# Kernel tuning notes

Hardware: AMD Instinct MI355X
Metric: run time of the kernel (lower is better)

The kernel has to match this reference:

```python
import jax, jax.numpy as jnp
import numpy as np

N = 100000      # nodes
E = 3_200_000   # edges
F_IN = 256      # input feature dim
R = 16          # rank_bound (GCN output dim)
D = 128         # embedding_dim (trans output)
B = 16384       # batch of node indices
EPS = 1e-5


def setup_inputs() -> dict:
    key = jax.random.key(0)
    ks = jax.random.split(key, 9)
    x = jax.random.normal(ks[0], (N, F_IN), jnp.float32)
    edge_index = jax.random.randint(ks[1], (2, E), 0, N, dtype=jnp.int64)
    trans = jax.random.normal(ks[2], (R, D), jnp.float32) * 0.1
    batch = jax.random.randint(ks[3], (B,), 0, N, dtype=jnp.int64)
    W = jax.random.normal(ks[4], (R, F_IN), jnp.float32) / np.sqrt(F_IN).astype(np.float32)
    b = jnp.zeros((R,), jnp.float32)
    ln_w = jnp.ones((R,), jnp.float32)
    ln_b = jnp.zeros((R,), jnp.float32)
    prelu_a = jnp.full((1,), 0.25, jnp.float32)  # PReLU single shared slope
    return dict(x=x, edge_index=edge_index, trans=trans, batch=batch,
                W=W, b=b, ln_w=ln_w, ln_b=ln_b, prelu_a=prelu_a)


def gcn_conv(x, edge_index, W, b):
    # PyG GCNConv: lin first, then symmetric-normalized aggregation with self-loops.
    h = x @ W.T  # [N, R]
    loop = jnp.arange(N, dtype=edge_index.dtype)
    src = jnp.concatenate([edge_index[0], loop])  # messages flow src -> dst
    dst = jnp.concatenate([edge_index[1], loop])
    deg = jax.ops.segment_sum(jnp.ones_like(dst, h.dtype), dst, num_segments=N)
    dinv = jnp.where(deg > 0, jax.lax.rsqrt(deg), 0.0)
    norm = dinv[src] * dinv[dst]                   # [E+N]
    msg = h[src] * norm[:, None]                   # gather [E+N, R]
    out = jax.ops.segment_sum(msg, dst, num_segments=N)  # scatter-add
    return out + b


def reference(x, edge_index, trans, batch, W, b, ln_w, ln_b, prelu_a):
    h = gcn_conv(x, edge_index, W, b)              # [N, R]
    # PyG LayerNorm (graph mode): normalize over all nodes and channels.
    h = h - h.mean()
    var = (h * h).mean()
    h = h * jax.lax.rsqrt(var + EPS) * ln_w + ln_b
    # PReLU
    h = jnp.where(h >= 0, h, prelu_a * h)
    emb = h @ trans                                # [N, D]
    return emb[batch]                              # index_select(0, batch)
```

## Files before the change

kernel.cpp:

```cpp
#include <hip/hip_runtime.h>

#define EPS 1e-5f
#define BSHIFT 8
#define BSIZE  256
#define NBMAX  512
#define PCHUNK 8192

__device__ __forceinline__ unsigned short f2bf(float f) {
    unsigned u = __float_as_uint(f);
    u += 0x7FFFu + ((u >> 16) & 1u);
    return (unsigned short)(u >> 16);
}
__device__ __forceinline__ float bf2f(unsigned short s) {
    return __uint_as_float(((unsigned)s) << 16);
}
__device__ __forceinline__ void acc8(float* acc, uint4 v) {
    acc[0] += bf2f((unsigned short)(v.x & 0xFFFFu)); acc[1] += bf2f((unsigned short)(v.x >> 16));
    acc[2] += bf2f((unsigned short)(v.y & 0xFFFFu)); acc[3] += bf2f((unsigned short)(v.y >> 16));
    acc[4] += bf2f((unsigned short)(v.z & 0xFFFFu)); acc[5] += bf2f((unsigned short)(v.z >> 16));
    acc[6] += bf2f((unsigned short)(v.w & 0xFFFFu)); acc[7] += bf2f((unsigned short)(v.w >> 16));
}

__global__ __launch_bounds__(512) void k_zero(unsigned* ghist, int NB) {
    int t = threadIdx.x;
    if (t < NB) ghist[t] = 0u;
}

__global__ __launch_bounds__(256) void k_bhist(const int* __restrict__ ei,
                                               unsigned* __restrict__ ghist, int E, int NB) {
    __shared__ unsigned sh[NBMAX];
    int t = threadIdx.x;
    for (int i = t; i < NB; i += 256) sh[i] = 0u;
    __syncthreads();
    const int4* dst4 = (const int4*)(ei + E);
    int E4 = E >> 2;
    int base4 = blockIdx.x * 1024;
#pragma unroll
    for (int i = 0; i < 4; i++) {
        int idx = base4 + i * 256 + t;
        if (idx < E4) {
            int4 d = dst4[idx];
            atomicAdd(&sh[d.x >> BSHIFT], 1u);
            atomicAdd(&sh[d.y >> BSHIFT], 1u);
            atomicAdd(&sh[d.z >> BSHIFT], 1u);
            atomicAdd(&sh[d.w >> BSHIFT], 1u);
        }
    }
    __syncthreads();
    for (int i = t; i < NB; i += 256) if (sh[i]) atomicAdd(&ghist[i], sh[i]);
}

__global__ __launch_bounds__(512) void k_bscan(const unsigned* __restrict__ ghist,
                                               unsigned* __restrict__ base,
                                               unsigned* __restrict__ cursor,
                                               unsigned* __restrict__ nstart,
                                               int NB, int N, int E) {
    __shared__ unsigned sh[512];
    int t = threadIdx.x;
    unsigned v = (t < NB) ? ghist[t] : 0u;
    sh[t] = v;
    __syncthreads();
    for (int off = 1; off < 512; off <<= 1) {
        unsigned a = (t >= off) ? sh[t - off] : 0u;
        __syncthreads();
        sh[t] += a;
        __syncthreads();
    }
    if (t < NB) { unsigned ex = sh[t] - v; base[t] = ex; cursor[t] = ex; }
    if (t == 0) { base[NB] = (unsigned)E; nstart[N] = (unsigned)E; }
}

__global__ __launch_bounds__(512) void k_bpart(const int* __restrict__ ei,
                                               unsigned* __restrict__ cursor,
                                               unsigned* __restrict__ sorted, int E, int NB) {
    __shared__ unsigned cnt[NBMAX];
    __shared__ unsigned lbase[NBMAX];
    __shared__ unsigned loff[NBMAX + 1];
    __shared__ unsigned sh[512];
    __shared__ unsigned stage[PCHUNK];
    __shared__ unsigned short bkt[PCHUNK];
    int t = threadIdx.x;
    for (int i = t; i < NB; i += 512) cnt[i] = 0u;
    __syncthreads();
    const int4* src4 = (const int4*)ei;
    const int4* dst4 = (const int4*)(ei + E);
    int E4 = E >> 2;
    int base4 = blockIdx.x * (PCHUNK / 4);
#pragma unroll
    for (int i = 0; i < PCHUNK / 4 / 512; i++) {
        int idx = base4 + i * 512 + t;
        if (idx < E4) {
            int4 d = dst4[idx];
            atomicAdd(&cnt[d.x >> BSHIFT], 1u);
            atomicAdd(&cnt[d.y >> BSHIFT], 1u);
            atomicAdd(&cnt[d.z >> BSHIFT], 1u);
            atomicAdd(&cnt[d.w >> BSHIFT], 1u);
        }
    }
    __syncthreads();
    unsigned v = (t < NB) ? cnt[t] : 0u;
    sh[t] = v;
    if (t < NB) lbase[t] = v ? atomicAdd(&cursor[t], v) : 0u;
    __syncthreads();
    for (int off = 1; off < 512; off <<= 1) {
        unsigned a = (t >= off) ? sh[t - off] : 0u;
        __syncthreads();
        sh[t] += a;
        __syncthreads();
    }
    if (t < NB) { loff[t] = sh[t] - v; cnt[t] = 0u; }
    if (t == NB - 1) loff[NB] = sh[t];
    __syncthreads();
    for (int b = t; b < NB; b += 512) {
        unsigned s = loff[b], e2 = loff[b + 1];
        for (unsigned j = s; j < e2; j++) bkt[j] = (unsigned short)b;
    }
#pragma unroll
    for (int i = 0; i < PCHUNK / 4 / 512; i++) {
        int idx = base4 + i * 512 + t;
        if (idx < E4) {
            int4 s = src4[idx];
            int4 d = dst4[idx];
            int b; unsigned r;
            b = d.x >> BSHIFT; r = atomicAdd(&cnt[b], 1u);
            stage[loff[b] + r] = (unsigned)s.x | ((unsigned)(d.x & (BSIZE - 1)) << 17);
            b = d.y >> BSHIFT; r = atomicAdd(&cnt[b], 1u);
            stage[loff[b] + r] = (unsigned)s.y | ((unsigned)(d.y & (BSIZE - 1)) << 17);
            b = d.z >> BSHIFT; r = atomicAdd(&cnt[b], 1u);
            stage[loff[b] + r] = (unsigned)s.z | ((unsigned)(d.z & (BSIZE - 1)) << 17);
            b = d.w >> BSHIFT; r = atomicAdd(&cnt[b], 1u);
            stage[loff[b] + r] = (unsigned)s.w | ((unsigned)(d.w & (BSIZE - 1)) << 17);
        }
    }
    __syncthreads();
    unsigned total = loff[NB];
    for (unsigned i = t; i < total; i += 512) {
        unsigned b = bkt[i];
        sorted[lbase[b] + (i - loff[b])] = stage[i];
    }
}

__global__ __launch_bounds__(256) void k_bdeg2(const unsigned* __restrict__ base,
                                               const unsigned* __restrict__ sorted,
                                               unsigned* __restrict__ nstart,
                                               float* __restrict__ dinv, int N) {
    __shared__ unsigned deg[BSIZE];
    int b = blockIdx.x, t = threadIdx.x;
    deg[t] = 0u;
    __syncthreads();
    unsigned s0 = base[b], s1 = base[b + 1];
    for (unsigned j = s0 + t; j < s1; j += 256)
        atomicAdd(&deg[sorted[j] >> 17], 1u);
    __syncthreads();
    unsigned d0 = deg[t];
    int lane = t & 63, wid = t >> 6;
    unsigned inc = d0;
    for (int off = 1; off < 64; off <<= 1) {
        unsigned u = __shfl_up(inc, off, 64);
        if (lane >= off) inc += u;
    }
    __shared__ unsigned wsum[4];
    if (lane == 63) wsum[wid] = inc;
    __syncthreads();
    unsigned wbase = 0;
    for (int w = 0; w < wid; w++) wbase += wsum[w];
    unsigned excl = wbase + inc - d0;
    int node = (b << BSHIFT) + t;
    if (node < N) {
        nstart[node] = s0 + excl;
        dinv[node] = rsqrtf((float)(d0 + 1u));
    }
}

__global__ __launch_bounds__(256) void k_bsort(const unsigned* __restrict__ base,
                                               const unsigned* __restrict__ nstart,
                                               const unsigned* __restrict__ sorted,
                                               unsigned* __restrict__ sorted2, int N) {
    __shared__ unsigned cur[BSIZE];
    int b = blockIdx.x, t = threadIdx.x;
    int node = (b << BSHIFT) + t;
    cur[t] = (node < N) ? nstart[node] : 0u;
    __syncthreads();
    unsigned s0 = base[b], s1 = base[b + 1];
    for (unsigned j = s0 + t; j < s1; j += 256) {
        unsigned u = sorted[j];
        unsigned pos = atomicAdd(&cur[u >> 17], 1u);
        sorted2[pos] = u & 0x1FFFFu;
    }
}

__global__ __launch_bounds__(256) void k_gemm(const float* __restrict__ x,
                                              const float* __restrict__ W,
                                              const float* __restrict__ dinv,
                                              unsigned short* __restrict__ hs, int N) {
    __shared__ float ws[16 * 256];
    int t = threadIdx.x;
    for (int i = t; i < 1024; i += 256) ((float4*)ws)[i] = ((const float4*)W)[i];
    __syncthreads();
    int node = blockIdx.x * 256 + t;
    if (node >= N) return;
    const float4* xr = (const float4*)(x + (size_t)node * 256);
    float acc[16];
#pragma unroll
    for (int r = 0; r < 16; r++) acc[r] = 0.f;
#pragma unroll 4
    for (int k = 0; k < 64; k++) {
        float4 a = xr[k];
#pragma unroll
        for (int r = 0; r < 16; r++) {
            float4 w = ((const float4*)ws)[r * 64 + k];
            acc[r] += a.x * w.x + a.y * w.y + a.z * w.z + a.w * w.w;
        }
    }
    float dv = dinv[node];
    unsigned pk[8];
#pragma unroll
    for (int i = 0; i < 8; i++)
        pk[i] = (unsigned)f2bf(acc[2 * i] * dv) | ((unsigned)f2bf(acc[2 * i + 1] * dv) << 16);
    uint4* dst = (uint4*)(hs + (size_t)node * 16);
    dst[0] = make_uint4(pk[0], pk[1], pk[2], pk[3]);
    dst[1] = make_uint4(pk[4], pk[5], pk[6], pk[7]);
}

__global__ __launch_bounds__(256) void k_agg3(const unsigned* __restrict__ nstart,
                                              const unsigned* __restrict__ sorted2,
                                              const unsigned short* __restrict__ hs,
                                              const float* __restrict__ dinv,
                                              const float* __restrict__ bias,
                                              float* __restrict__ agg,
                                              float2* __restrict__ part, int N) {
    int t = threadIdx.x;
    int g = t >> 4, r = t & 15;
    int d = blockIdx.x * 16 + g;
    int sub = r >> 1;
    int half = r & 1;
    float acc[8];
#pragma unroll
    for (int c = 0; c < 8; c++) acc[c] = 0.f;
    unsigned s0 = 0, s1 = 0;
    if (d < N) { s0 = nstart[d]; s1 = nstart[d + 1]; }
    for (unsigned j = s0; j < s1; j += 16) {
        unsigned row0 = j + sub, row1 = j + 8 + sub;
        bool p0 = row0 < s1, p1 = row1 < s1;
        unsigned i0 = 0, i1 = 0;
        if (p0) i0 = sorted2[row0];
        if (p1) i1 = sorted2[row1];
        uint4 v0, v1;
        if (p0) v0 = ((const uint4*)(hs + (size_t)i0 * 16))[half];
        if (p1) v1 = ((const uint4*)(hs + (size_t)i1 * 16))[half];
        if (p0) acc8(acc, v0);
        if (p1) acc8(acc, v1);
    }
#pragma unroll
    for (int off = 2; off <= 8; off <<= 1) {
#pragma unroll
        for (int c = 0; c < 8; c++) acc[c] += __shfl_down(acc[c], off, 64);
    }
    float s = 0.f, q = 0.f;
    if (d < N && r < 2) {
        float dd = dinv[d];
        uint4 hv = ((const uint4*)(hs + (size_t)d * 16))[half];
        float self[8];
        self[0] = bf2f((unsigned short)(hv.x & 0xFFFFu)); self[1] = bf2f((unsigned short)(hv.x >> 16));
        self[2] = bf2f((unsigned short)(hv.y & 0xFFFFu)); self[3] = bf2f((unsigned short)(hv.y >> 16));
        self[4] = bf2f((unsigned short)(hv.z & 0xFFFFu)); self[5] = bf2f((unsigned short)(hv.z >> 16));
        self[6] = bf2f((unsigned short)(hv.w & 0xFFFFu)); self[7] = bf2f((unsigned short)(hv.w >> 16));
        float o[8];
#pragma unroll
        for (int c = 0; c < 8; c++) o[c] = (acc[c] + self[c]) * dd;
        float* an = agg + (size_t)d * 16 + half * 8;
        *(float4*)(an)     = make_float4(o[0], o[1], o[2], o[3]);
        *(float4*)(an + 4) = make_float4(o[4], o[5], o[6], o[7]);
        const float* bp = bias + half * 8;
        float4 b0 = *(const float4*)bp, b1 = *(const float4*)(bp + 4);
        float a0 = o[0] + b0.x, a1 = o[1] + b0.y, a2 = o[2] + b0.z, a3 = o[3] + b0.w;
        float a4 = o[4] + b1.x, a5 = o[5] + b1.y, a6 = o[6] + b1.z, a7 = o[7] + b1.w;
        s = (a0 + a1) + (a2 + a3) + (a4 + a5) + (a6 + a7);
        q = a0 * a0 + a1 * a1 + a2 * a2 + a3 * a3 + a4 * a4 + a5 * a5 + a6 * a6 + a7 * a7;
    }
    for (int off = 32; off > 0; off >>= 1) {
        s += __shfl_down(s, off, 64);
        q += __shfl_down(q, off, 64);
    }
    __shared__ float ss[4], qq[4];
    int lane = t & 63, wid = t >> 6;
    if (lane == 0) { ss[wid] = s; qq[wid] = q; }
    __syncthreads();
    if (t == 0)
        part[blockIdx.x] = make_float2(ss[0] + ss[1] + ss[2] + ss[3],
                                       qq[0] + qq[1] + qq[2] + qq[3]);
}

__global__ __launch_bounds__(256) void k_statsred(const float2* __restrict__ part,
                                                  float* __restrict__ scal, int M) {
    int t = threadIdx.x;
    float s = 0.f, q = 0.f;
    for (int i = t; i < M; i += 256) {
        float2 v = part[i];
        s += v.x; q += v.y;
    }
    for (int off = 32; off > 0; off >>= 1) {
        s += __shfl_down(s, off, 64);
        q += __shfl_down(q, off, 64);
    }
    __shared__ float ss[4], qq[4];
    int lane = t & 63, wid = t >> 6;
    if (lane == 0) { ss[wid] = s; qq[wid] = q; }
    __syncthreads();
    if (t == 0) {
        scal[0] = ss[0] + ss[1] + ss[2] + ss[3];
        scal[1] = qq[0] + qq[1] + qq[2] + qq[3];
    }
}

__global__ __launch_bounds__(256) void k_final(const float* __restrict__ agg,
                                               const int* __restrict__ batch,
                                               const float* __restrict__ trans,
                                               const float* __restrict__ bias,
                                               const float* __restrict__ ln_w,
                                               const float* __restrict__ ln_b,
                                               const float* __restrict__ prelu_a,
                                               const float* __restrict__ scal,
                                               float* __restrict__ out, int B, float invCnt) {
    __shared__ float tl[16 * 128];
    __shared__ float hh[2 * 16];
    const int tid = threadIdx.x;
    for (int i = tid; i < 2048; i += 256) tl[i] = trans[i];
    float mean = scal[0] * invCnt;
    float var  = scal[1] * invCnt - mean * mean;
    float inv  = rsqrtf(var + EPS);
    int row0 = blockIdx.x * 2;
    if (tid < 32) {
        int lr = tid >> 4, r = tid & 15;
        int row = row0 + lr;
        if (row < B) {
            int node = batch[row];
            float v = agg[(size_t)node * 16 + r] + bias[r];
            v = (v - mean) * inv * ln_w[r] + ln_b[r];
            float a = prelu_a[0];
            v = v >= 0.f ? v : a * v;
            hh[lr * 16 + r] = v;
        }
    }
    __syncthreads();
    int lr = tid >> 7, d = tid & 127;
    int row = row0 + lr;
    if (row >= B) return;
    const float* hrow = hh + lr * 16;
    float acc = 0.f;
#pragma unroll
    for (int r = 0; r < 16; r++) acc += hrow[r] * tl[r * 128 + d];
    out[(size_t)row * 128 + d] = acc;
}

extern "C" void kernel_launch(void* const* d_in, const int* in_sizes, int n_in,
                              void* d_out, int out_size, void* d_ws, size_t ws_size,
                              hipStream_t stream) {
    const float* x       = (const float*)d_in[0];
    const int*   ei      = (const int*)d_in[1];
    const float* trans   = (const float*)d_in[2];
    const int*   batch   = (const int*)d_in[3];
    const float* W       = (const float*)d_in[4];
    const float* bias    = (const float*)d_in[5];
    const float* ln_w    = (const float*)d_in[6];
    const float* ln_b    = (const float*)d_in[7];
    const float* prelu_a = (const float*)d_in[8];
    float* out = (float*)d_out;

    const int N = in_sizes[0] / 256;
    const int E = in_sizes[1] / 2;
    const int B = in_sizes[3];
    const int NB = (N + BSIZE - 1) >> BSHIFT;
    const int NBLK = (N + 15) / 16;

    char* p = (char*)d_ws;
    unsigned short* hs = (unsigned short*)p;  p += (size_t)N * 16 * 2;
    float*    agg     = (float*)p;     p += (size_t)N * 16 * 4;
    unsigned* sorted  = (unsigned*)p;  p += (size_t)E * 4;
    unsigned* sorted2 = (unsigned*)p;  p += (size_t)E * 4;
    float*    dinv    = (float*)p;     p += (size_t)N * 4;
    unsigned* nstart  = (unsigned*)p;  p += (size_t)(N + 1) * 4;
    unsigned* ghist   = (unsigned*)p;  p += NBMAX * 4;
    unsigned* base    = (unsigned*)p;  p += (NBMAX + 1) * 4;
    unsigned* cursor  = (unsigned*)p;  p += NBMAX * 4;
    float*    scal    = (float*)p;     p += 2 * 4;
    p = (char*)(((size_t)p + 7) & ~(size_t)7);
    float2*   part    = (float2*)p;    p += (size_t)NBLK * 8;

    int E4 = E >> 2;
    int pbh = (E4 + 1023) / 1024;
    int pbp = (E + PCHUNK - 1) / PCHUNK;

    hipLaunchKernelGGL(k_zero,     dim3(1),               dim3(512), 0, stream, ghist, NB);
    hipLaunchKernelGGL(k_bhist,    dim3(pbh),             dim3(256), 0, stream, ei, ghist, E, NB);
    hipLaunchKernelGGL(k_bscan,    dim3(1),               dim3(512), 0, stream, ghist, base, cursor, nstart, NB, N, E);
    hipLaunchKernelGGL(k_bpart,    dim3(pbp),             dim3(512), 0, stream, ei, cursor, sorted, E, NB);
    hipLaunchKernelGGL(k_bdeg2,    dim3(NB),              dim3(256), 0, stream, base, sorted, nstart, dinv, N);
    hipLaunchKernelGGL(k_bsort,    dim3(NB),              dim3(256), 0, stream, base, nstart, sorted, sorted2, N);
    hipLaunchKernelGGL(k_gemm,     dim3((N + 255) / 256), dim3(256), 0, stream, x, W, dinv, hs, N);
    hipLaunchKernelGGL(k_agg3,     dim3(NBLK),            dim3(256), 0, stream, nstart, sorted2, hs, dinv, bias, agg, part, N);
    hipLaunchKernelGGL(k_statsred, dim3(1),               dim3(256), 0, stream, part, scal, NBLK);
    hipLaunchKernelGGL(k_final,    dim3((B + 1) / 2),     dim3(256), 0, stream, agg, batch, trans, bias,
                       ln_w, ln_b, prelu_a, scal, out, B, 1.0f / (float)(N * 16));
}
```

Measured before the change: 322.3 us.

## Fuse per-node sort into aggregation via LDS and reuse per-block histograms

The histogram kernel now records per-block bucket counts so the partition kernel no longer re-reads destinations and recounts them. The separate per-node sort kernel is removed. Aggregation now runs one block per 256-node bucket, scatters that bucket's edges into an LDS buffer (with a global scratch fallback), then aggregates 16 nodes per pass. The final kernel processes 8 batch rows per block with trans columns held in registers. This saves a global write and read of the sorted edge array and one launch, at the cost of only 1 block per 256 nodes (about 391 blocks), which lowers parallelism in the gather phase and uses 48KB of LDS per block, limiting occupancy.

```diff
diff --git a/kernel.cpp b/kernel.cpp
--- a/kernel.cpp
+++ b/kernel.cpp
@@ -5,6 +5,7 @@
 #define BSIZE  256
 #define NBMAX  512
 #define PCHUNK 8192
+#define LCAP   12288
 
 __device__ __forceinline__ unsigned short f2bf(float f) {
     unsigned u = __float_as_uint(f);
@@ -26,18 +27,20 @@
     if (t < NB) ghist[t] = 0u;
 }
 
-__global__ __launch_bounds__(256) void k_bhist(const int* __restrict__ ei,
-                                               unsigned* __restrict__ ghist, int E, int NB) {
+__global__ __launch_bounds__(512) void k_bhist(const int* __restrict__ ei,
+                                               unsigned* __restrict__ ghist,
+                                               unsigned* __restrict__ blkhist,
+                                               int E, int NB) {
     __shared__ unsigned sh[NBMAX];
     int t = threadIdx.x;
-    for (int i = t; i < NB; i += 256) sh[i] = 0u;
+    for (int i = t; i < NB; i += 512) sh[i] = 0u;
     __syncthreads();
     const int4* dst4 = (const int4*)(ei + E);
     int E4 = E >> 2;
-    int base4 = blockIdx.x * 1024;
-#pragma unroll
-    for (int i = 0; i < 4; i++) {
-        int idx = base4 + i * 256 + t;
+    int base4 = blockIdx.x * (PCHUNK / 4);
+#pragma unroll
+    for (int i = 0; i < PCHUNK / 4 / 512; i++) {
+        int idx = base4 + i * 512 + t;
         if (idx < E4) {
             int4 d = dst4[idx];
             atomicAdd(&sh[d.x >> BSHIFT], 1u);
@@ -47,7 +50,12 @@
         }
     }
     __syncthreads();
-    for (int i = t; i < NB; i += 256) if (sh[i]) atomicAdd(&ghist[i], sh[i]);
+    unsigned* bh = blkhist + (size_t)blockIdx.x * NBMAX;
+    for (int i = t; i < NB; i += 512) {
+        unsigned c = sh[i];
+        bh[i] = c;
+        if (c) atomicAdd(&ghist[i], c);
+    }
 }
 
 __global__ __launch_bounds__(512) void k_bscan(const unsigned* __restrict__ ghist,
@@ -71,6 +79,7 @@
 }
 
 __global__ __launch_bounds__(512) void k_bpart(const int* __restrict__ ei,
+                                               const unsigned* __restrict__ blkhist,
                                                unsigned* __restrict__ cursor,
                                                unsigned* __restrict__ sorted, int E, int NB) {
     __shared__ unsigned cnt[NBMAX];
@@ -80,24 +89,13 @@
     __shared__ unsigned stage[PCHUNK];
     __shared__ unsigned short bkt[PCHUNK];
     int t = threadIdx.x;
-    for (int i = t; i < NB; i += 512) cnt[i] = 0u;
+    const unsigned* bh = blkhist + (size_t)blockIdx.x * NBMAX;
+    for (int i = t; i < NB; i += 512) cnt[i] = bh[i];
     __syncthreads();
     const int4* src4 = (const int4*)ei;
     const int4* dst4 = (const int4*)(ei + E);
     int E4 = E >> 2;
     int base4 = blockIdx.x * (PCHUNK / 4);
-#pragma unroll
-    for (int i = 0; i < PCHUNK / 4 / 512; i++) {
-        int idx = base4 + i * 512 + t;
-        if (idx < E4) {
-            int4 d = dst4[idx];
-            atomicAdd(&cnt[d.x >> BSHIFT], 1u);
-            atomicAdd(&cnt[d.y >> BSHIFT], 1u);
-            atomicAdd(&cnt[d.z >> BSHIFT], 1u);
-            atomicAdd(&cnt[d.w >> BSHIFT], 1u);
-        }
-    }
-    __syncthreads();
     unsigned v = (t < NB) ? cnt[t] : 0u;
     sh[t] = v;
     if (t < NB) lbase[t] = v ? atomicAdd(&cursor[t], v) : 0u;
@@ -172,23 +170,6 @@
     }
 }
 
-__global__ __launch_bounds__(256) void k_bsort(const unsigned* __restrict__ base,
-                                               const unsigned* __restrict__ nstart,
-                                               const unsigned* __restrict__ sorted,
-                                               unsigned* __restrict__ sorted2, int N) {
-    __shared__ unsigned cur[BSIZE];
-    int b = blockIdx.x, t = threadIdx.x;
-    int node = (b << BSHIFT) + t;
-    cur[t] = (node < N) ? nstart[node] : 0u;
-    __syncthreads();
-    unsigned s0 = base[b], s1 = base[b + 1];
-    for (unsigned j = s0 + t; j < s1; j += 256) {
-        unsigned u = sorted[j];
-        unsigned pos = atomicAdd(&cur[u >> 17], 1u);
-        sorted2[pos] = u & 0x1FFFFu;
-    }
-}
-
 __global__ __launch_bounds__(256) void k_gemm(const float* __restrict__ x,
                                               const float* __restrict__ W,
                                               const float* __restrict__ dinv,
@@ -222,73 +203,111 @@
     dst[1] = make_uint4(pk[4], pk[5], pk[6], pk[7]);
 }
 
-__global__ __launch_bounds__(256) void k_agg3(const unsigned* __restrict__ nstart,
-                                              const unsigned* __restrict__ sorted2,
+__global__ __launch_bounds__(256) void k_aggf(const unsigned* __restrict__ base,
+                                              const unsigned* __restrict__ nstart,
+                                              const unsigned* __restrict__ sorted,
                                               const unsigned short* __restrict__ hs,
                                               const float* __restrict__ dinv,
                                               const float* __restrict__ bias,
                                               float* __restrict__ agg,
-                                              float2* __restrict__ part, int N) {
-    int t = threadIdx.x;
+                                              float2* __restrict__ part,
+                                              unsigned* __restrict__ scratch, int N) {
+    __shared__ unsigned buf[LCAP];
+    __shared__ unsigned cur0[BSIZE + 1];
+    __shared__ unsigned curv[BSIZE];
+    __shared__ float ss[4], qq[4];
+    int b = blockIdx.x, t = threadIdx.x;
+    unsigned s0 = base[b], s1 = base[b + 1];
+    unsigned len = s1 - s0;
+    int node = (b << BSHIFT) + t;
+    unsigned ns = (node < N) ? nstart[node] : s1;
+    cur0[t] = ns - s0;
+    curv[t] = ns - s0;
+    if (t == 0) cur0[BSIZE] = len;
+    __syncthreads();
+    bool fit = (len <= (unsigned)LCAP);
+    if (fit) {
+        for (unsigned j = t; j < len; j += 256) {
+            unsigned u = sorted[s0 + j];
+            unsigned pos = atomicAdd(&curv[u >> 17], 1u);
+            buf[pos] = u & 0x1FFFFu;
+        }
+    } else {
+        for (unsigned j = t; j < len; j += 256) {
+            unsigned u = sorted[s0 + j];
+            unsigned pos = atomicAdd(&curv[u >> 17], 1u);
+            scratch[s0 + pos] = u & 0x1FFFFu;
+        }
+    }
+    __syncthreads();
     int g = t >> 4, r = t & 15;
-    int d = blockIdx.x * 16 + g;
     int sub = r >> 1;
     int half = r & 1;
-    float acc[8];
-#pragma unroll
-    for (int c = 0; c < 8; c++) acc[c] = 0.f;
-    unsigned s0 = 0, s1 = 0;
-    if (d < N) { s0 = nstart[d]; s1 = nstart[d + 1]; }
-    for (unsigned j = s0; j < s1; j += 16) {
-        unsigned row0 = j + sub, row1 = j + 8 + sub;
-        bool p0 = row0 < s1, p1 = row1 < s1;
-        unsigned i0 = 0, i1 = 0;
-        if (p0) i0 = sorted2[row0];
-        if (p1) i1 = sorted2[row1];
-        uint4 v0, v1;
-        if (p0) v0 = ((const uint4*)(hs + (size_t)i0 * 16))[half];
-        if (p1) v1 = ((const uint4*)(hs + (size_t)i1 * 16))[half];
-        if (p0) acc8(acc, v0);
-        if (p1) acc8(acc, v1);
-    }
-#pragma unroll
-    for (int off = 2; off <= 8; off <<= 1) {
-#pragma unroll
-        for (int c = 0; c < 8; c++) acc[c] += __shfl_down(acc[c], off, 64);
-    }
-    float s = 0.f, q = 0.f;
-    if (d < N && r < 2) {
-        float dd = dinv[d];
-        uint4 hv = ((const uint4*)(hs + (size_t)d * 16))[half];
-        float self[8];
-        self[0] = bf2f((unsigned short)(hv.x & 0xFFFFu)); self[1] = bf2f((unsigned short)(hv.x >> 16));
-        self[2] = bf2f((unsigned short)(hv.y & 0xFFFFu)); self[3] = bf2f((unsigned short)(hv.y >> 16));
-        self[4] = bf2f((unsigned short)(hv.z & 0xFFFFu)); self[5] = bf2f((unsigned short)(hv.z >> 16));
-        self[6] = bf2f((unsigned short)(hv.w & 0xFFFFu)); self[7] = bf2f((unsigned short)(hv.w >> 16));
-        float o[8];
-#pragma unroll
-        for (int c = 0; c < 8; c++) o[c] = (acc[c] + self[c]) * dd;
-        float* an = agg + (size_t)d * 16 + half * 8;
-        *(float4*)(an)     = make_float4(o[0], o[1], o[2], o[3]);
-        *(float4*)(an + 4) = make_float4(o[4], o[5], o[6], o[7]);
-        const float* bp = bias + half * 8;
-        float4 b0 = *(const float4*)bp, b1 = *(const float4*)(bp + 4);
-        float a0 = o[0] + b0.x, a1 = o[1] + b0.y, a2 = o[2] + b0.z, a3 = o[3] + b0.w;
-        float a4 = o[4] + b1.x, a5 = o[5] + b1.y, a6 = o[6] + b1.z, a7 = o[7] + b1.w;
-        s = (a0 + a1) + (a2 + a3) + (a4 + a5) + (a6 + a7);
-        q = a0 * a0 + a1 * a1 + a2 * a2 + a3 * a3 + a4 * a4 + a5 * a5 + a6 * a6 + a7 * a7;
+    float sacc = 0.f, qacc = 0.f;
+#pragma unroll 1
+    for (int p = 0; p < 16; p++) {
+        int dloc = p * 16 + g;
+        int d = (b << BSHIFT) + dloc;
+        float acc[8];
+#pragma unroll
+        for (int c = 0; c < 8; c++) acc[c] = 0.f;
+        if (d < N) {
+            unsigned l0 = cur0[dloc], l1 = cur0[dloc + 1];
+            for (unsigned j = l0; j < l1; j += 16) {
+                unsigned row0 = j + sub, row1 = j + 8 + sub;
+                bool p0 = row0 < l1, p1 = row1 < l1;
+                unsigned i0 = 0, i1 = 0;
+                if (fit) {
+                    if (p0) i0 = buf[row0];
+                    if (p1) i1 = buf[row1];
+                } else {
+                    if (p0) i0 = scratch[s0 + row0];
+                    if (p1) i1 = scratch[s0 + row1];
+                }
+                uint4 v0, v1;
+                if (p0) v0 = ((const uint4*)(hs + (size_t)i0 * 16))[half];
+                if (p1) v1 = ((const uint4*)(hs + (size_t)i1 * 16))[half];
+                if (p0) acc8(acc, v0);
+                if (p1) acc8(acc, v1);
+            }
+        }
+#pragma unroll
+        for (int off = 2; off <= 8; off <<= 1) {
+#pragma unroll
+            for (int c = 0; c < 8; c++) acc[c] += __shfl_down(acc[c], off, 64);
+        }
+        if (d < N && r < 2) {
+            float dd = dinv[d];
+            uint4 hv = ((const uint4*)(hs + (size_t)d * 16))[half];
+            float self[8];
+            self[0] = bf2f((unsigned short)(hv.x & 0xFFFFu)); self[1] = bf2f((unsigned short)(hv.x >> 16));
+            self[2] = bf2f((unsigned short)(hv.y & 0xFFFFu)); self[3] = bf2f((unsigned short)(hv.y >> 16));
+            self[4] = bf2f((unsigned short)(hv.z & 0xFFFFu)); self[5] = bf2f((unsigned short)(hv.z >> 16));
+            self[6] = bf2f((unsigned short)(hv.w & 0xFFFFu)); self[7] = bf2f((unsigned short)(hv.w >> 16));
+            float o[8];
+#pragma unroll
+            for (int c = 0; c < 8; c++) o[c] = (acc[c] + self[c]) * dd;
+            float* an = agg + (size_t)d * 16 + half * 8;
+            *(float4*)(an)     = make_float4(o[0], o[1], o[2], o[3]);
+            *(float4*)(an + 4) = make_float4(o[4], o[5], o[6], o[7]);
+            const float* bp = bias + half * 8;
+            float4 b0 = *(const float4*)bp, b1 = *(const float4*)(bp + 4);
+            float a0 = o[0] + b0.x, a1 = o[1] + b0.y, a2 = o[2] + b0.z, a3 = o[3] + b0.w;
+            float a4 = o[4] + b1.x, a5 = o[5] + b1.y, a6 = o[6] + b1.z, a7 = o[7] + b1.w;
+            sacc += (a0 + a1) + (a2 + a3) + (a4 + a5) + (a6 + a7);
+            qacc += a0 * a0 + a1 * a1 + a2 * a2 + a3 * a3 + a4 * a4 + a5 * a5 + a6 * a6 + a7 * a7;
+        }
     }
     for (int off = 32; off > 0; off >>= 1) {
-        s += __shfl_down(s, off, 64);
-        q += __shfl_down(q, off, 64);
-    }
-    __shared__ float ss[4], qq[4];
+        sacc += __shfl_down(sacc, off, 64);
+        qacc += __shfl_down(qacc, off, 64);
+    }
     int lane = t & 63, wid = t >> 6;
-    if (lane == 0) { ss[wid] = s; qq[wid] = q; }
+    if (lane == 0) { ss[wid] = sacc; qq[wid] = qacc; }
     __syncthreads();
     if (t == 0)
-        part[blockIdx.x] = make_float2(ss[0] + ss[1] + ss[2] + ss[3],
-                                       qq[0] + qq[1] + qq[2] + qq[3]);
+        part[b] = make_float2(ss[0] + ss[1] + ss[2] + ss[3],
+                              qq[0] + qq[1] + qq[2] + qq[3]);
 }
 
 __global__ __launch_bounds__(256) void k_statsred(const float2* __restrict__ part,
@@ -323,14 +342,14 @@
                                                const float* __restrict__ scal,
                                                float* __restrict__ out, int B, float invCnt) {
     __shared__ float tl[16 * 128];
-    __shared__ float hh[2 * 16];
+    __shared__ float hh[8 * 16];
     const int tid = threadIdx.x;
     for (int i = tid; i < 2048; i += 256) tl[i] = trans[i];
     float mean = scal[0] * invCnt;
     float var  = scal[1] * invCnt - mean * mean;
     float inv  = rsqrtf(var + EPS);
-    int row0 = blockIdx.x * 2;
-    if (tid < 32) {
+    int row0 = blockIdx.x * 8;
+    if (tid < 128) {
         int lr = tid >> 4, r = tid & 15;
         int row = row0 + lr;
         if (row < B) {
@@ -343,14 +362,22 @@
         }
     }
     __syncthreads();
-    int lr = tid >> 7, d = tid & 127;
-    int row = row0 + lr;
-    if (row >= B) return;
-    const float* hrow = hh + lr * 16;
-    float acc = 0.f;
-#pragma unroll
-    for (int r = 0; r < 16; r++) acc += hrow[r] * tl[r * 128 + d];
-    out[(size_t)row * 128 + d] = acc;
+    int d = tid & 127, hlf = tid >> 7;
+    float tv[16];
+#pragma unroll
+    for (int r = 0; r < 16; r++) tv[r] = tl[r * 128 + d];
+#pragma unroll
+    for (int rr = 0; rr < 4; rr++) {
+        int lr = rr * 2 + hlf;
+        int row = row0 + lr;
+        if (row < B) {
+            const float* hrow = hh + lr * 16;
+            float acc = 0.f;
+#pragma unroll
+            for (int r = 0; r < 16; r++) acc += hrow[r] * tv[r];
+            out[(size_t)row * 128 + d] = acc;
+        }
+    }
 }
 
 extern "C" void kernel_launch(void* const* d_in, const int* in_sizes, int n_in,
@@ -371,13 +398,14 @@
     const int E = in_sizes[1] / 2;
     const int B = in_sizes[3];
     const int NB = (N + BSIZE - 1) >> BSHIFT;
-    const int NBLK = (N + 15) / 16;
+    const int pbp = (E + PCHUNK - 1) / PCHUNK;
 
     char* p = (char*)d_ws;
     unsigned short* hs = (unsigned short*)p;  p += (size_t)N * 16 * 2;
     float*    agg     = (float*)p;     p += (size_t)N * 16 * 4;
     unsigned* sorted  = (unsigned*)p;  p += (size_t)E * 4;
-    unsigned* sorted2 = (unsigned*)p;  p += (size_t)E * 4;
+    unsigned* scratch = (unsigned*)p;  p += (size_t)E * 4;
+    unsigned* blkhist = (unsigned*)p;  p += (size_t)pbp * NBMAX * 4;
     float*    dinv    = (float*)p;     p += (size_t)N * 4;
     unsigned* nstart  = (unsigned*)p;  p += (size_t)(N + 1) * 4;
     unsigned* ghist   = (unsigned*)p;  p += NBMAX * 4;
@@ -385,21 +413,16 @@
     unsigned* cursor  = (unsigned*)p;  p += NBMAX * 4;
     float*    scal    = (float*)p;     p += 2 * 4;
     p = (char*)(((size_t)p + 7) & ~(size_t)7);
-    float2*   part    = (float2*)p;    p += (size_t)NBLK * 8;
-
-    int E4 = E >> 2;
-    int pbh = (E4 + 1023) / 1024;
-    int pbp = (E + PCHUNK - 1) / PCHUNK;
+    float2*   part    = (float2*)p;    p += (size_t)NB * 8;
 
     hipLaunchKernelGGL(k_zero,     dim3(1),               dim3(512), 0, stream, ghist, NB);
-    hipLaunchKernelGGL(k_bhist,    dim3(pbh),             dim3(256), 0, stream, ei, ghist, E, NB);
+    hipLaunchKernelGGL(k_bhist,    dim3(pbp),             dim3(512), 0, stream, ei, ghist, blkhist, E, NB);
     hipLaunchKernelGGL(k_bscan,    dim3(1),               dim3(512), 0, stream, ghist, base, cursor, nstart, NB, N, E);
-    hipLaunchKernelGGL(k_bpart,    dim3(pbp),             dim3(512), 0, stream, ei, cursor, sorted, E, NB);
+    hipLaunchKernelGGL(k_bpart,    dim3(pbp),             dim3(512), 0, stream, ei, blkhist, cursor, sorted, E, NB);
     hipLaunchKernelGGL(k_bdeg2,    dim3(NB),              dim3(256), 0, stream, base, sorted, nstart, dinv, N);
-    hipLaunchKernelGGL(k_bsort,    dim3(NB),              dim3(256), 0, stream, base, nstart, sorted, sorted2, N);
     hipLaunchKernelGGL(k_gemm,     dim3((N + 255) / 256), dim3(256), 0, stream, x, W, dinv, hs, N);
-    hipLaunchKernelGGL(k_agg3,     dim3(NBLK),            dim3(256), 0, stream, nstart, sorted2, hs, dinv, bias, agg, part, N);
-    hipLaunchKernelGGL(k_statsred, dim3(1),               dim3(256), 0, stream, part, scal, NBLK);
-    hipLaunchKernelGGL(k_final,    dim3((B + 1) / 2),     dim3(256), 0, stream, agg, batch, trans, bias,
+    hipLaunchKernelGGL(k_aggf,     dim3(NB),              dim3(256), 0, stream, base, nstart, sorted, hs, dinv, bias, agg, part, scratch, N);
+    hipLaunchKernelGGL(k_statsred, dim3(1),               dim3(256), 0, stream, part, scal, NB);
+    hipLaunchKernelGGL(k_final,    dim3((B + 7) / 8),     dim3(256), 0, stream, agg, batch, trans, bias,
                        ln_w, ln_b, prelu_a, scal, out, B, 1.0f / (float)(N * 16));
 }
```

New measurement: 302.4 us. 6.2% less time.
